# Kernel optimization log

Measured on AMD Instinct MI355X. Metric: run time of the kernel, lower is better.

## Reference

```python
import jax, jax.numpy as jnp
import numpy as np
import math

B, T, J, D2 = 32, 512, 43, 2
DM, H, FF, E, NC = 512, 8, 2048, 101, 100  # d_model, heads, ffn, n_experts(=max_output_len+1), classes


def _ln(x, g, b, eps=1e-5):
    mu = x.mean(-1, keepdims=True)
    var = ((x - mu) ** 2).mean(-1, keepdims=True)
    return (x - mu) / jnp.sqrt(var + eps) * g + b


def _pos_encoding(t, d):
    pos = jnp.arange(t, dtype=jnp.float32)[:, None]
    div = jnp.exp(jnp.arange(0, d, 2, dtype=jnp.float32) * (-math.log(10000.0) / d))
    pe = jnp.zeros((t, d), dtype=jnp.float32)
    pe = pe.at[:, 0::2].set(jnp.sin(pos * div))
    pe = pe.at[:, 1::2].set(jnp.cos(pos * div))
    return pe


def _mha(x, qkv_w, qkv_b, ow, ob, heads):
    b_, t_, d_ = x.shape
    dh = d_ // heads
    qkv = x @ qkv_w.T + qkv_b
    q, k, v = jnp.split(qkv, 3, axis=-1)
    sh = lambda a: a.reshape(b_, t_, heads, dh).transpose(0, 2, 1, 3)
    q, k, v = sh(q), sh(k), sh(v)
    s = jnp.einsum('bhqd,bhkd->bhqk', q, k) / jnp.sqrt(jnp.asarray(dh, x.dtype))
    a = jax.nn.softmax(s, axis=-1)
    ctx = jnp.einsum('bhqk,bhkd->bhqd', a, v).transpose(0, 2, 1, 3).reshape(b_, t_, d_)
    return ctx @ ow.T + ob


def _conv1d(x, w, b):  # x: [B,C,T], w: [O,I,3]
    y = jax.lax.conv_general_dilated(x, w, (1,), [(1, 1)], dimension_numbers=('NCH', 'OIH', 'NCH'))
    return y + b[None, :, None]


def _avgpool2(x):  # [B,C,T] -> [B,C,T//2]
    b_, c_, t_ = x.shape
    return x.reshape(b_, c_, t_ // 2, 2).mean(-1)


def _expert(pos, qkv_w, qkv_b, ow, ob, ng, nb, lw, lb, memory):
    m = memory + pos  # pos: [D], broadcast over [B,Tp,D]
    out = _mha(m, qkv_w, qkv_b, ow, ob, heads=1)
    c = out.mean(axis=1)           # [B,D]
    c = _ln(c, ng, nb)
    return c @ lw.T + lb           # [B,D]


_experts_vmapped = jax.vmap(_expert, in_axes=(0,) * 9 + (None,))


def _forward(poses, W_in, b_in,
             eq_w, eq_b, eo_w, eo_b, ef1_w, ef1_b, ef2_w, ef2_b,
             en1_g, en1_b, en2_g, en2_b,
             c1_w, c1_b, c2_w, c2_b, mlp_w, mlp_b,
             xp_pos, xp_qkv_w, xp_qkv_b, xp_o_w, xp_o_b, xp_n_g, xp_n_b, xp_l_w, xp_l_b,
             fn_g, fn_b, hd_w, hd_b):
    b_, t_, j_, d2_ = poses.shape
    x = poses.reshape(b_, t_, j_ * d2_)
    x = x @ W_in.T + b_in                          # [B,T,DM]
    x = x + _pos_encoding(t_, DM)[None]
    # 2-layer post-norm transformer encoder (torch default: relu FFN, norm after residual)
    for i in range(2):
        a = _mha(x, eq_w[i], eq_b[i], eo_w[i], eo_b[i], heads=H)
        x = _ln(x + a, en1_g[i], en1_b[i])
        ff = jax.nn.relu(x @ ef1_w[i].T + ef1_b[i]) @ ef2_w[i].T + ef2_b[i]
        x = _ln(x + ff, en2_g[i], en2_b[i])
    # temporal pooling: conv-gelu-pool x2  -> [B,DM,T/4]
    y = x.transpose(0, 2, 1)
    y = _avgpool2(jax.nn.gelu(_conv1d(y, c1_w, c1_b), approximate=False))
    y = _avgpool2(jax.nn.gelu(_conv1d(y, c2_w, c2_b), approximate=False))
    mem = y.transpose(0, 2, 1)                      # [B,T/4,DM]
    mem = jax.nn.gelu(mem @ mlp_w.T + mlp_b, approximate=False)
    # all position experts in one batched call: [E,B,DM]
    ctx = _experts_vmapped(xp_pos, xp_qkv_w, xp_qkv_b, xp_o_w, xp_o_b,
                           xp_n_g, xp_n_b, xp_l_w, xp_l_b, mem)
    ctx = _ln(ctx, fn_g, fn_b)
    logits = ctx @ hd_w.T + hd_b                    # [E,B,NC]
    return logits.transpose(1, 0, 2)                # [B,E,NC]


def setup_inputs() -> dict:
    key = jax.random.key(0)
    ks = iter(jax.random.split(key, 64))
    nrm = lambda shape, s=0.02: jax.random.normal(next(ks), shape, dtype=jnp.float32) * s
    inp = {
        'poses': jax.random.normal(next(ks), (B, T, J, D2), dtype=jnp.float32),
        'W_in': nrm((DM, J * D2)), 'b_in': jnp.zeros((DM,)),
        'eq_w': nrm((2, 3 * DM, DM)), 'eq_b': jnp.zeros((2, 3 * DM)),
        'eo_w': nrm((2, DM, DM)), 'eo_b': jnp.zeros((2, DM)),
        'ef1_w': nrm((2, FF, DM)), 'ef1_b': jnp.zeros((2, FF)),
        'ef2_w': nrm((2, DM, FF)), 'ef2_b': jnp.zeros((2, DM)),
        'en1_g': jnp.ones((2, DM)), 'en1_b': jnp.zeros((2, DM)),
        'en2_g': jnp.ones((2, DM)), 'en2_b': jnp.zeros((2, DM)),
        'c1_w': nrm((DM, DM, 3)), 'c1_b': jnp.zeros((DM,)),
        'c2_w': nrm((DM, DM, 3)), 'c2_b': jnp.zeros((DM,)),
        'mlp_w': nrm((DM, DM)), 'mlp_b': jnp.zeros((DM,)),
        'xp_pos': nrm((E, DM)),
        'xp_qkv_w': nrm((E, 3 * DM, DM)), 'xp_qkv_b': jnp.zeros((E, 3 * DM)),
        'xp_o_w': nrm((E, DM, DM)), 'xp_o_b': jnp.zeros((E, DM)),
        'xp_n_g': jnp.ones((E, DM)), 'xp_n_b': jnp.zeros((E, DM)),
        'xp_l_w': nrm((E, DM, DM)), 'xp_l_b': jnp.zeros((E, DM)),
        'fn_g': jnp.ones((DM,)), 'fn_b': jnp.zeros((DM,)),
        'hd_w': nrm((NC, DM)), 'hd_b': jnp.zeros((NC,)),
    }
    return inp


def reference(poses, W_in, b_in,
              eq_w, eq_b, eo_w, eo_b, ef1_w, ef1_b, ef2_w, ef2_b,
              en1_g, en1_b, en2_g, en2_b,
              c1_w, c1_b, c2_w, c2_b, mlp_w, mlp_b,
              xp_pos, xp_qkv_w, xp_qkv_b, xp_o_w, xp_o_b, xp_n_g, xp_n_b, xp_l_w, xp_l_b,
              fn_g, fn_b, hd_w, hd_b):
    return _forward(poses, W_in, b_in,
                    eq_w, eq_b, eo_w, eo_b, ef1_w, ef1_b, ef2_w, ef2_b,
                    en1_g, en1_b, en2_g, en2_b,
                    c1_w, c1_b, c2_w, c2_b, mlp_w, mlp_b,
                    xp_pos, xp_qkv_w, xp_qkv_b, xp_o_w, xp_o_b, xp_n_g, xp_n_b, xp_l_w, xp_l_b,
                    fn_g, fn_b, hd_w, hd_b)
```

## Files before the change

### kernel.cpp

```cpp
#include <hip/hip_runtime.h>
#include <math.h>

typedef unsigned short u16;
typedef __bf16 bf16_t;
typedef bf16_t bf16x8 __attribute__((ext_vector_type(8)));
typedef float f32x4v __attribute__((ext_vector_type(4)));
typedef u16 u16x8 __attribute__((ext_vector_type(8)));
typedef u16 u16x4 __attribute__((ext_vector_type(4)));

__device__ inline u16 f2bf(float f){ __bf16 h=(__bf16)f; return __builtin_bit_cast(u16,h); }
__device__ inline float bf2f(u16 u){ unsigned int x=((unsigned int)u)<<16; return __builtin_bit_cast(float,x); }

#define GLD16(gp,lp) __builtin_amdgcn_global_load_lds( \
  (const __attribute__((address_space(1))) void*)(gp), \
  (__attribute__((address_space(3))) void*)(lp), 16, 0, 0)

#define MFMA_B16(a,b,c) __builtin_amdgcn_mfma_f32_16x16x32_bf16(a,b,c,0,0,0)
#define ALPHA_S 0.044194173824159216f

struct GP {
  const u16* A; int lda; long long sA1, sA2;
  const u16* B; int ldb; long long sB1, sB2;
  const float* bias; long long sb1, sb2, sbg;
  float* Cf; u16* Cb; int ldc; long long sC1, sC2;
  int M, N, K, Z2, epi, perm;
  float alpha;
};

__device__ inline float epiF(float v,int epi){
  if(epi==1) return fmaxf(v,0.f);
  if(epi==2) return 0.5f*v*(1.f+erff(v*0.70710678118654752f));
  return v;
}

__global__ __launch_bounds__(256) void gemm_bt(GP p){
  __shared__ u16 L[3*8192];
  const int z=blockIdx.z, z1=z/p.Z2, z2=z-z1*p.Z2;
  const u16* __restrict__ Ab = p.A + z1*p.sA1 + z2*p.sA2;
  const u16* __restrict__ Bb = p.B + z1*p.sB1 + z2*p.sB2;
  const int tm=blockIdx.x*128, tn=blockIdx.y*128;
  const int t=threadIdx.x, lane=t&63, wv=t>>6;
  const int wr=(wv>>1)*64, wc=(wv&1)*64;
  const int fr=lane&15, c16=lane>>4;

  long long aoff[2], boff[2];
  #pragma unroll
  for(int q=0;q<2;q++){
    int s=(wv*2+q)*64+lane;
    int r=s>>2;
    int col=((s&3)^((r>>1)&3))*8;
    int ga=tm+r; if(ga>p.M-1) ga=p.M-1;
    int gb=tn+r; if(gb>p.N-1) gb=p.N-1;
    aoff[q]=(long long)ga*p.lda+col;
    boff[q]=(long long)gb*p.ldb+col;
  }

  auto STAGE=[&](int tk,int buf){
    const long long kk=(long long)tk*32;
    u16* base=&L[buf*8192];
    #pragma unroll
    for(int q=0;q<2;q++){
      GLD16(Ab+aoff[q]+kk, base+(wv*2+q)*512);
      GLD16(Bb+boff[q]+kk, base+4096+(wv*2+q)*512);
    }
  };

  const int nt = p.K >> 5;
  f32x4v acc[4][4]={};

  STAGE(0,0);
  if(nt>1){
    STAGE(1,1);
    asm volatile("s_waitcnt vmcnt(4)" ::: "memory");
  } else {
    asm volatile("s_waitcnt vmcnt(0)" ::: "memory");
  }
  __builtin_amdgcn_s_barrier();
  __builtin_amdgcn_sched_barrier(0);

  for(int i=0;i<nt;++i){
    const int buf=i%3;
    if(i+2<nt) STAGE(i+2,(i+2)%3);
    const u16* Abuf=&L[buf*8192];
    const u16* Bbuf=&L[buf*8192+4096];
    bf16x8 af[4], bfv[4];
    #pragma unroll
    for(int m=0;m<4;m++){ int r=wr+16*m+fr; af[m]=*(const bf16x8*)&Abuf[r*32+((c16^((r>>1)&3))*8)]; }
    #pragma unroll
    for(int n=0;n<4;n++){ int r=wc+16*n+fr; bfv[n]=*(const bf16x8*)&Bbuf[r*32+((c16^((r>>1)&3))*8)]; }
    #pragma unroll
    for(int m=0;m<4;m++)
      #pragma unroll
      for(int n=0;n<4;n++)
        acc[m][n]=MFMA_B16(af[m],bfv[n],acc[m][n]);
    if(i+1<nt){
      if(i+2<nt) asm volatile("s_waitcnt vmcnt(4)" ::: "memory");
      else       asm volatile("s_waitcnt vmcnt(0)" ::: "memory");
      __builtin_amdgcn_s_barrier();
      __builtin_amdgcn_sched_barrier(0);
    }
  }

  const int rq=lane>>4;
  const long long cbase = z1*p.sC1 + z2*p.sC2;
  float* __restrict__ Cf = p.Cf? p.Cf+cbase : nullptr;
  u16*  __restrict__ Cbp = p.Cb? p.Cb+cbase : nullptr;

  const bool vec = (!p.perm) && (p.epi!=3) && ((p.N&63)==0) && !(Cf&&Cbp);
  if(vec){
    float bvn[4];
    #pragma unroll
    for(int n=0;n<4;n++){
      int gc=tn+wc+n*16+fr; if(gc>p.N-1) gc=p.N-1;
      bvn[n]=p.bias? p.bias[z1*p.sb1+z2*p.sb2+(long long)gc*p.sbg] : 0.f;
    }
    if(Cbp){
      u16* my=(u16*)L + wv*1024;
      #pragma unroll
      for(int m=0;m<4;m++){
        __syncthreads();
        #pragma unroll
        for(int n=0;n<4;n++){
          int pg=((n^rq)<<4)+fr;
          #pragma unroll
          for(int r=0;r<4;r++)
            my[(4*rq+r)*64+pg]=f2bf(epiF(acc[m][n][r]*p.alpha+bvn[n],p.epi));
        }
        __syncthreads();
        #pragma unroll
        for(int ps=0;ps<2;ps++){
          int row=ps*8+(lane>>3), h=lane&7;
          int grow=tm+wr+m*16+row, gc0=tn+wc+h*8;
          if(grow<p.M && gc0<p.N){
            int phys=(((h>>1)^(row>>2))<<4)+((h&1)<<3);
            *(u16x8*)&Cbp[(long long)grow*p.ldc+gc0]=*(const u16x8*)&my[row*64+phys];
          }
        }
      }
    } else {
      float* my=(float*)L + wv*1024;
      #pragma unroll
      for(int m=0;m<4;m++){
        __syncthreads();
        #pragma unroll
        for(int n=0;n<4;n++){
          int pg=((n^rq)<<4)+fr;
          #pragma unroll
          for(int r=0;r<4;r++)
            my[(4*rq+r)*64+pg]=epiF(acc[m][n][r]*p.alpha+bvn[n],p.epi);
        }
        __syncthreads();
        #pragma unroll
        for(int ps=0;ps<2;ps++){
          int row=ps*8+(lane>>3), h=lane&7;
          int grow=tm+wr+m*16+row, gc0=tn+wc+h*8;
          if(grow<p.M && gc0<p.N){
            int phys=(((h>>1)^(row>>2))<<4)+((h&1)<<3);
            *(float4*)&Cf[(long long)grow*p.ldc+gc0]  =*(const float4*)&my[row*64+phys];
            *(float4*)&Cf[(long long)grow*p.ldc+gc0+4]=*(const float4*)&my[row*64+phys+4];
          }
        }
      }
    }
    return;
  }

  #pragma unroll
  for(int m=0;m<4;m++){
    int grow0=tm+wr+16*m+4*rq;
    #pragma unroll
    for(int n=0;n<4;n++){
      int gcol=tn+wc+16*n+fr;
      if(gcol>=p.N) continue;
      float bv = p.bias? p.bias[z1*p.sb1+z2*p.sb2+(long long)gcol*p.sbg] : 0.f;
      #pragma unroll
      for(int r=0;r<4;r++){
        int grow=grow0+r;
        if(grow>=p.M) continue;
        float v=acc[m][n][r]*p.alpha+bv;
        if(p.epi==1) v=fmaxf(v,0.f);
        else if(p.epi==2) v=0.5f*v*(1.f+erff(v*0.70710678118654752f));
        else if(p.epi==3){
          int tt=grow&511;
          float ang=(float)tt*expf((float)(gcol&~1)*(-0.017988946039015967f));
          v += (gcol&1)? cosf(ang) : sinf(ang);
        }
        long long ci;
        if(p.perm) ci = ((long long)((grow&31)*101 + (grow>>5)))*100 + gcol;
        else       ci = (long long)grow*p.ldc+gcol;
        if(Cf) Cf[ci]=v;
        if(Cbp) Cbp[ci]=f2bf(v);
      }
    }
  }
}

__global__ __launch_bounds__(256) void gemm_sfused(
    const u16* __restrict__ Pm, const u16* __restrict__ mem,
    const float* __restrict__ U, float* __restrict__ abar){
  __shared__ float Sl[128*129];
  u16* L=(u16*)Sl;
  const int z=blockIdx.x, e=z>>5, b=z&31;
  const u16* __restrict__ Ab = Pm + (long long)e*2097152 + (long long)b*65536;
  const u16* __restrict__ Bb = mem + (long long)b*65536;
  const int t=threadIdx.x, lane=t&63, wv=t>>6;
  const int wr=(wv>>1)*64, wc=(wv&1)*64;
  const int fr=lane&15, c16=lane>>4;

  long long aoff[2], boff[2];
  #pragma unroll
  for(int q=0;q<2;q++){
    int s=(wv*2+q)*64+lane;
    int r=s>>2;
    int col=((s&3)^((r>>1)&3))*8;
    aoff[q]=(long long)r*512+col;
    boff[q]=(long long)r*512+col;
  }
  auto STAGE=[&](int tk,int buf){
    const long long kk=(long long)tk*32;
    u16* base=&L[buf*8192];
    #pragma unroll
    for(int q=0;q<2;q++){
      GLD16(Ab+aoff[q]+kk, base+(wv*2+q)*512);
      GLD16(Bb+boff[q]+kk, base+4096+(wv*2+q)*512);
    }
  };

  f32x4v acc[4][4]={};
  STAGE(0,0);
  STAGE(1,1);
  asm volatile("s_waitcnt vmcnt(4)" ::: "memory");
  __builtin_amdgcn_s_barrier();
  __builtin_amdgcn_sched_barrier(0);

  for(int i=0;i<16;++i){
    const int buf=i%3;
    if(i+2<16) STAGE(i+2,(i+2)%3);
    const u16* Abuf=&L[buf*8192];
    const u16* Bbuf=&L[buf*8192+4096];
    bf16x8 af[4], bfv[4];
    #pragma unroll
    for(int m=0;m<4;m++){ int r=wr+16*m+fr; af[m]=*(const bf16x8*)&Abuf[r*32+((c16^((r>>1)&3))*8)]; }
    #pragma unroll
    for(int n=0;n<4;n++){ int r=wc+16*n+fr; bfv[n]=*(const bf16x8*)&Bbuf[r*32+((c16^((r>>1)&3))*8)]; }
    #pragma unroll
    for(int m=0;m<4;m++)
      #pragma unroll
      for(int n=0;n<4;n++)
        acc[m][n]=MFMA_B16(af[m],bfv[n],acc[m][n]);
    if(i+1<16){
      if(i+2<16) asm volatile("s_waitcnt vmcnt(4)" ::: "memory");
      else       asm volatile("s_waitcnt vmcnt(0)" ::: "memory");
      __builtin_amdgcn_s_barrier();
      __builtin_amdgcn_sched_barrier(0);
    }
  }

  const int rq=lane>>4;
  float bvn[4];
  #pragma unroll
  for(int n=0;n<4;n++){
    int col=wc+n*16+fr;
    bvn[n]=U[((long long)(b*128+col))*101+e];
  }
  __syncthreads();
  #pragma unroll
  for(int m=0;m<4;m++)
    #pragma unroll
    for(int n=0;n<4;n++){
      int col=wc+n*16+fr;
      #pragma unroll
      for(int r=0;r<4;r++){
        int row=wr+m*16+4*rq+r;
        Sl[row*129+col]=acc[m][n][r]*ALPHA_S+bvn[n];
      }
    }
  __syncthreads();
  {
    int row=t>>1, h=t&1;
    float* pr=&Sl[row*129+h*64];
    float mx=pr[0];
    for(int j=1;j<64;j++) mx=fmaxf(mx,pr[j]);
    mx=fmaxf(mx,__shfl_xor(mx,1));
    float s=0.f;
    for(int j=0;j<64;j++){ float ex=__expf(pr[j]-mx); pr[j]=ex; s+=ex; }
    s+=__shfl_xor(s,1);
    float inv=1.f/s;
    for(int j=0;j<64;j++) pr[j]*=inv;
  }
  __syncthreads();
  if(t<128){
    float s=0.f;
    for(int r=0;r<128;r++) s+=Sl[r*129+t];
    abar[(long long)z*128+t]=s*(1.f/128.f);
  }
}

__global__ __launch_bounds__(512) void gemm_big8(GP p){
  __shared__ u16 L[65536];
  const int z=blockIdx.z, z1=z/p.Z2, z2=z-z1*p.Z2;
  const u16* __restrict__ Ab = p.A + z1*p.sA1 + z2*p.sA2;
  const u16* __restrict__ Bb = p.B + z1*p.sB1 + z2*p.sB2;
  const int tm=blockIdx.x*256, tn=blockIdx.y*256;
  const int t=threadIdx.x, lane=t&63, wv=t>>6;
  const int wr2=(wv>>2)*128, wc2=(wv&3)*64;
  const int fr=lane&15, c16=lane>>4;

  long long aoff[2], boff[2];
  {
    int rr=t>>2, cs=((t&3)^((t>>3)&3))*8;
    #pragma unroll
    for(int q=0;q<2;q++){
      int ga=tm+q*128+rr; if(ga>p.M-1) ga=p.M-1;
      int gb=tn+q*128+rr; if(gb>p.N-1) gb=p.N-1;
      aoff[q]=(long long)ga*p.lda+cs;
      boff[q]=(long long)gb*p.ldb+cs;
    }
  }

  auto STAGE_A=[&](int kt,int d,int ks){
    const long long k0=(long long)kt*64+ks*32;
    u16* dst=&L[d*16384+ks*8192];
    GLD16(Ab+aoff[0]+k0, dst+t*8);
    GLD16(Ab+aoff[1]+k0, dst+4096+t*8);
  };
  auto STAGE_B=[&](int kt,int d,int ks){
    const long long k0=(long long)kt*64+ks*32;
    u16* dst=&L[32768+d*16384+ks*8192];
    GLD16(Bb+boff[0]+k0, dst+t*8);
    GLD16(Bb+boff[1]+k0, dst+4096+t*8);
  };
  auto LDA_=[&](int d,int ks,int m)->bf16x8{
    int R=wr2+m*16+fr;
    return *(const bf16x8*)&L[d*16384+ks*8192+R*32+((c16^((R>>1)&3))*8)];
  };
  auto LDB_=[&](int d,int ks,int n)->bf16x8{
    int R=wc2+n*16+fr;
    return *(const bf16x8*)&L[32768+d*16384+ks*8192+R*32+((c16^((R>>1)&3))*8)];
  };

  const int ntk=p.K>>6;
  f32x4v acc[8][4]={};
  bf16x8 af[8], bq0, bq1, bq2, bq3;

  STAGE_A(0,0,0); STAGE_B(0,0,0); STAGE_A(0,0,1); STAGE_B(0,0,1);
  asm volatile("s_waitcnt vmcnt(4)" ::: "memory");
  __builtin_amdgcn_s_barrier();
  __builtin_amdgcn_sched_barrier(0);

  for(int kt=0;kt<ntk;++kt){
    const int d=kt&1, nd=d^1;
    const bool nxt=(kt+1<ntk);
    #pragma unroll
    for(int m=0;m<8;m++) af[m]=LDA_(d,0,m);
    bq0=LDB_(d,0,0); bq1=LDB_(d,0,1);
    if(nxt) STAGE_A(kt+1,nd,0);
    __builtin_amdgcn_s_barrier();
    asm volatile("s_waitcnt lgkmcnt(0)" ::: "memory");
    __builtin_amdgcn_sched_barrier(0);
    __builtin_amdgcn_s_setprio(1);
    #pragma unroll
    for(int m=0;m<8;m++){
      acc[m][0]=MFMA_B16(af[m],bq0,acc[m][0]);
      acc[m][1]=MFMA_B16(af[m],bq1,acc[m][1]);
    }
    __builtin_amdgcn_s_setprio(0);
    __builtin_amdgcn_s_barrier();
    bq2=LDB_(d,0,2); bq3=LDB_(d,0,3);
    if(nxt) STAGE_B(kt+1,nd,0);
    __builtin_amdgcn_s_barrier();
    asm volatile("s_waitcnt lgkmcnt(0)" ::: "memory");
    __builtin_amdgcn_sched_barrier(0);
    __builtin_amdgcn_s_setprio(1);
    #pragma unroll
    for(int m=0;m<8;m++){
      acc[m][2]=MFMA_B16(af[m],bq2,acc[m][2]);
      acc[m][3]=MFMA_B16(af[m],bq3,acc[m][3]);
    }
    __builtin_amdgcn_s_setprio(0);
    if(nxt) asm volatile("s_waitcnt vmcnt(4)" ::: "memory");
    else    asm volatile("s_waitcnt vmcnt(0)" ::: "memory");
    __builtin_amdgcn_s_barrier();
    __builtin_amdgcn_sched_barrier(0);
    #pragma unroll
    for(int m=0;m<8;m++) af[m]=LDA_(d,1,m);
    bq0=LDB_(d,1,0); bq1=LDB_(d,1,1);
    if(nxt) STAGE_A(kt+1,nd,1);
    __builtin_amdgcn_s_barrier();
    asm volatile("s_waitcnt lgkmcnt(0)" ::: "memory");
    __builtin_amdgcn_sched_barrier(0);
    __builtin_amdgcn_s_setprio(1);
    #pragma unroll
    for(int m=0;m<8;m++){
      acc[m][0]=MFMA_B16(af[m],bq0,acc[m][0]);
      acc[m][1]=MFMA_B16(af[m],bq1,acc[m][1]);
    }
    __builtin_amdgcn_s_setprio(0);
    __builtin_amdgcn_s_barrier();
    bq2=LDB_(d,1,2); bq3=LDB_(d,1,3);
    if(nxt) STAGE_B(kt+1,nd,1);
    __builtin_amdgcn_s_barrier();
    asm volatile("s_waitcnt lgkmcnt(0)" ::: "memory");
    __builtin_amdgcn_sched_barrier(0);
    __builtin_amdgcn_s_setprio(1);
    #pragma unroll
    for(int m=0;m<8;m++){
      acc[m][2]=MFMA_B16(af[m],bq2,acc[m][2]);
      acc[m][3]=MFMA_B16(af[m],bq3,acc[m][3]);
    }
    __builtin_amdgcn_s_setprio(0);
    if(nxt) asm volatile("s_waitcnt vmcnt(4)" ::: "memory");
    __builtin_amdgcn_s_barrier();
    __builtin_amdgcn_sched_barrier(0);
  }

  const int rq=lane>>4;
  const long long cbase = z1*p.sC1 + z2*p.sC2;
  float* __restrict__ Cf = p.Cf? p.Cf+cbase : nullptr;
  u16*  __restrict__ Cbp = p.Cb? p.Cb+cbase : nullptr;

  const bool vec = (!p.perm) && (p.epi!=3) && ((p.N&63)==0) && !(Cf&&Cbp);
  if(vec){
    float bvn[4];
    #pragma unroll
    for(int n=0;n<4;n++){
      int gc=tn+wc2+n*16+fr; if(gc>p.N-1) gc=p.N-1;
      bvn[n]=p.bias? p.bias[z1*p.sb1+z2*p.sb2+(long long)gc*p.sbg] : 0.f;
    }
    if(Cbp){
      u16* my=(u16*)L + wv*1024;
      #pragma unroll
      for(int m=0;m<8;m++){
        __syncthreads();
        #pragma unroll
        for(int n=0;n<4;n++){
          int pg=((n^rq)<<4)+fr;
          #pragma unroll
          for(int r=0;r<4;r++)
            my[(4*rq+r)*64+pg]=f2bf(epiF(acc[m][n][r]*p.alpha+bvn[n],p.epi));
        }
        __syncthreads();
        #pragma unroll
        for(int ps=0;ps<2;ps++){
          int row=ps*8+(lane>>3), h=lane&7;
          int grow=tm+wr2+m*16+row, gc0=tn+wc2+h*8;
          if(grow<p.M && gc0<p.N){
            int phys=(((h>>1)^(row>>2))<<4)+((h&1)<<3);
            *(u16x8*)&Cbp[(long long)grow*p.ldc+gc0]=*(const u16x8*)&my[row*64+phys];
          }
        }
      }
    } else {
      float* my=(float*)L + wv*1024;
      #pragma unroll
      for(int m=0;m<8;m++){
        __syncthreads();
        #pragma unroll
        for(int n=0;n<4;n++){
          int pg=((n^rq)<<4)+fr;
          #pragma unroll
          for(int r=0;r<4;r++)
            my[(4*rq+r)*64+pg]=epiF(acc[m][n][r]*p.alpha+bvn[n],p.epi);
        }
        __syncthreads();
        #pragma unroll
        for(int ps=0;ps<2;ps++){
          int row=ps*8+(lane>>3), h=lane&7;
          int grow=tm+wr2+m*16+row, gc0=tn+wc2+h*8;
          if(grow<p.M && gc0<p.N){
            int phys=(((h>>1)^(row>>2))<<4)+((h&1)<<3);
            *(float4*)&Cf[(long long)grow*p.ldc+gc0]  =*(const float4*)&my[row*64+phys];
            *(float4*)&Cf[(long long)grow*p.ldc+gc0+4]=*(const float4*)&my[row*64+phys+4];
          }
        }
      }
    }
    return;
  }

  #pragma unroll
  for(int m=0;m<8;m++){
    int grow0=tm+wr2+m*16+4*rq;
    #pragma unroll
    for(int n=0;n<4;n++){
      int gcol=tn+wc2+n*16+fr;
      if(gcol>=p.N) continue;
      float bv = p.bias? p.bias[z1*p.sb1+z2*p.sb2+gcol] : 0.f;
      #pragma unroll
      for(int r=0;r<4;r++){
        int grow=grow0+r;
        if(grow>=p.M) continue;
        float v=epiF(acc[m][n][r]*p.alpha+bv,p.epi);
        long long ci=(long long)grow*p.ldc+gcol;
        if(Cf) Cf[ci]=v;
        if(Cbp) Cbp[ci]=f2bf(v);
      }
    }
  }
}

__global__ __launch_bounds__(256) void softmax512b(u16* __restrict__ S, int nrows){
  int row=blockIdx.x*4+(threadIdx.x>>6);
  if(row>=nrows) return;
  int lane=threadIdx.x&63;
  u16* p=S+(long long)row*512;
  u16x8 raw=*(u16x8*)&p[lane*8];
  float f[8];
  #pragma unroll
  for(int j=0;j<8;j++) f[j]=bf2f(raw[j]);
  float m=f[0];
  #pragma unroll
  for(int j=1;j<8;j++) m=fmaxf(m,f[j]);
  #pragma unroll
  for(int off=32;off;off>>=1) m=fmaxf(m,__shfl_xor(m,off));
  float s=0.f;
  #pragma unroll
  for(int j=0;j<8;j++){ f[j]=__expf(f[j]-m); s+=f[j]; }
  #pragma unroll
  for(int off=32;off;off>>=1) s+=__shfl_xor(s,off);
  float inv=1.f/s;
  u16x8 o;
  #pragma unroll
  for(int j=0;j<8;j++) o[j]=f2bf(f[j]*inv);
  *(u16x8*)&p[lane*8]=o;
}

__global__ __launch_bounds__(256) void ln512(
    const float* __restrict__ x, const float* __restrict__ res,
    const float* __restrict__ g, const float* __restrict__ bb, int pergroup,
    float* __restrict__ outf, u16* __restrict__ outb, int nrows)
{
  int row=blockIdx.x*4+(threadIdx.x>>6);
  if(row>=nrows) return;
  int lane=threadIdx.x&63;
  const float4* xp=(const float4*)(x+(long long)row*512);
  float4 v0=xp[lane], v1=xp[lane+64];
  if(res){
    const float4* rp=(const float4*)(res+(long long)row*512);
    float4 w0=rp[lane], w1=rp[lane+64];
    v0.x+=w0.x; v0.y+=w0.y; v0.z+=w0.z; v0.w+=w0.w;
    v1.x+=w1.x; v1.y+=w1.y; v1.z+=w1.z; v1.w+=w1.w;
  }
  float s=v0.x+v0.y+v0.z+v0.w+v1.x+v1.y+v1.z+v1.w;
  #pragma unroll
  for(int off=32;off;off>>=1) s+=__shfl_xor(s,off);
  float mu=s*(1.f/512.f);
  float q=(v0.x-mu)*(v0.x-mu)+(v0.y-mu)*(v0.y-mu)+(v0.z-mu)*(v0.z-mu)+(v0.w-mu)*(v0.w-mu)
        +(v1.x-mu)*(v1.x-mu)+(v1.y-mu)*(v1.y-mu)+(v1.z-mu)*(v1.z-mu)+(v1.w-mu)*(v1.w-mu);
  #pragma unroll
  for(int off=32;off;off>>=1) q+=__shfl_xor(q,off);
  float rstd=rsqrtf(q*(1.f/512.f)+1e-5f);
  long long go = pergroup? (long long)(row>>5)*512 : 0;
  float4 g0=((const float4*)(g+go))[lane],  g1=((const float4*)(g+go))[lane+64];
  float4 b0=((const float4*)(bb+go))[lane], b1=((const float4*)(bb+go))[lane+64];
  float4 o0,o1;
  o0.x=(v0.x-mu)*rstd*g0.x+b0.x; o0.y=(v0.y-mu)*rstd*g0.y+b0.y;
  o0.z=(v0.z-mu)*rstd*g0.z+b0.z; o0.w=(v0.w-mu)*rstd*g0.w+b0.w;
  o1.x=(v1.x-mu)*rstd*g1.x+b1.x; o1.y=(v1.y-mu)*rstd*g1.y+b1.y;
  o1.z=(v1.z-mu)*rstd*g1.z+b1.z; o1.w=(v1.w-mu)*rstd*g1.w+b1.w;
  if(outf){
    ((float4*)(outf+(long long)row*512))[lane]=o0;
    ((float4*)(outf+(long long)row*512))[lane+64]=o1;
  }
  if(outb){
    u16x4 h0,h1;
    h0[0]=f2bf(o0.x); h0[1]=f2bf(o0.y); h0[2]=f2bf(o0.z); h0[3]=f2bf(o0.w);
    h1[0]=f2bf(o1.x); h1[1]=f2bf(o1.y); h1[2]=f2bf(o1.z); h1[3]=f2bf(o1.w);
    ((u16x4*)(outb+(long long)row*512))[lane]=h0;
    ((u16x4*)(outb+(long long)row*512))[lane+64]=h1;
  }
}

__global__ __launch_bounds__(256) void vtransb(const u16* __restrict__ qkv,
                                               u16* __restrict__ Vt){
  __shared__ u16 tile[64][72];
  int tt=blockIdx.x, h=blockIdx.y, zb=blockIdx.z;
  int t=threadIdx.x;
  int i=t>>2, j0=(t&3)*16;
  const u16* src = qkv + ((long long)(zb*512 + tt*64 + i))*1536 + 1024 + h*64 + j0;
  *(u16x8*)&tile[i][j0]   = *(const u16x8*)&src[0];
  *(u16x8*)&tile[i][j0+8] = *(const u16x8*)&src[8];
  __syncthreads();
  int j=t>>2, i0=(t&3)*16;
  u16 tmp[16];
  #pragma unroll
  for(int c=0;c<16;c++) tmp[c]=tile[i0+c][j];
  u16* dst = Vt + ((long long)((zb*8+h)*64 + j))*512 + tt*64 + i0;
  *(u16x8*)&dst[0]=*(u16x8*)&tmp[0];
  *(u16x8*)&dst[8]=*(u16x8*)&tmp[8];
}

__global__ __launch_bounds__(256) void trcvtb(const float* __restrict__ src,
                                              u16* __restrict__ dst){
  __shared__ float tile[64][65];
  int bi=blockIdx.x, bj=blockIdx.y, z=blockIdx.z;
  int e=z>>1, half=z&1;
  const float* s = src + (long long)e*786432 + half*262144;
  int t=threadIdx.x;
  int i=t>>2, j0=(t&3)*16;
  const float* sp = s + (long long)(bi*64+i)*512 + bj*64 + j0;
  #pragma unroll
  for(int c=0;c<4;c++){
    float4 v=((const float4*)sp)[c];
    tile[i][j0+4*c+0]=v.x; tile[i][j0+4*c+1]=v.y;
    tile[i][j0+4*c+2]=v.z; tile[i][j0+4*c+3]=v.w;
  }
  __syncthreads();
  int j=t>>2, i0=(t&3)*16;
  u16* d = dst + (long long)z*262144 + (long long)(bj*64+j)*512 + bi*64 + i0;
  u16x8 o0,o1;
  #pragma unroll
  for(int c=0;c<8;c++){ o0[c]=f2bf(tile[i0+c][j]); o1[c]=f2bf(tile[i0+8+c][j]); }
  *(u16x8*)&d[0]=o0; *(u16x8*)&d[8]=o1;
}

__global__ __launch_bounds__(256) void im2col3b(const u16* __restrict__ in,
                                                u16* __restrict__ out,
                                                int Tlen, long long n8){
  long long idx=(long long)blockIdx.x*256+threadIdx.x;
  if(idx>=n8) return;
  int i8=(int)(idx&63); long long s=idx>>6;
  int dt=(int)(s%3); long long bt=s/3;
  int tt=(int)(bt%Tlen); int b=(int)(bt/Tlen);
  int tsrc=tt+dt-1;
  u16x8 v={0,0,0,0,0,0,0,0};
  if(tsrc>=0 && tsrc<Tlen) v=*(const u16x8*)&in[((long long)(b*Tlen+tsrc))*512 + i8*8];
  *(u16x8*)&out[idx*8]=v;
}

__global__ __launch_bounds__(256) void wrepackb(const float* __restrict__ w,
                                                u16* __restrict__ out){
  int idx=blockIdx.x*256+threadIdx.x;
  if(idx>=512*1536) return;
  int o=idx/1536; int rem=idx-o*1536;
  int dt=rem/512; int i=rem-dt*512;
  out[idx]=f2bf(w[((long long)o*512+i)*3+dt]);
}

__global__ __launch_bounds__(256) void pool2b(const float* __restrict__ in,
                                              u16* __restrict__ out,
                                              int Tlen, long long n4){
  long long idx=(long long)blockIdx.x*256+threadIdx.x;
  if(idx>=n4) return;
  int c=(int)((idx&127)*4); long long s=idx>>7;
  int half=Tlen/2;
  int tp=(int)(s%half); int b=(int)(s/half);
  const float* p=in+((long long)(b*Tlen+2*tp))*512+c;
  float4 a=*(const float4*)p, d=*(const float4*)(p+512);
  u16x4 o;
  o[0]=f2bf(0.5f*(a.x+d.x)); o[1]=f2bf(0.5f*(a.y+d.y));
  o[2]=f2bf(0.5f*(a.z+d.z)); o[3]=f2bf(0.5f*(a.w+d.w));
  *(u16x4*)&out[(s*512)+c]=o;
}

__global__ __launch_bounds__(256) void cvt_bf16(const float* __restrict__ in,
                                                u16* __restrict__ out, long long n8){
  long long i=(long long)blockIdx.x*256+threadIdx.x;
  if(i>=n8) return;
  const float4* p=(const float4*)(in+i*8);
  float4 a=p[0], b=p[1];
  u16x8 o;
  o[0]=f2bf(a.x); o[1]=f2bf(a.y); o[2]=f2bf(a.z); o[3]=f2bf(a.w);
  o[4]=f2bf(b.x); o[5]=f2bf(b.y); o[6]=f2bf(b.z); o[7]=f2bf(b.w);
  *(u16x8*)(out+i*8)=o;
}

__global__ __launch_bounds__(256) void cvt_wv(const float* __restrict__ in,
                                              u16* __restrict__ out, long long n8){
  long long idx=(long long)blockIdx.x*256+threadIdx.x;
  if(idx>=n8) return;
  int e=(int)(idx>>15); long long r8=idx&32767;
  const float* p=in+(long long)e*786432+524288+r8*8;
  float4 a=((const float4*)p)[0], b=((const float4*)p)[1];
  u16x8 o;
  o[0]=f2bf(a.x); o[1]=f2bf(a.y); o[2]=f2bf(a.z); o[3]=f2bf(a.w);
  o[4]=f2bf(b.x); o[5]=f2bf(b.y); o[6]=f2bf(b.z); o[7]=f2bf(b.w);
  *(u16x8*)(out+idx*8)=o;
}

__global__ __launch_bounds__(256) void cvt_pad(const float* __restrict__ in,
                                               u16* __restrict__ out,
                                               int rows, int ks, int kd){
  long long idx=(long long)blockIdx.x*256+threadIdx.x;
  if(idx>=(long long)rows*kd) return;
  int r=(int)(idx/kd), c=(int)(idx-(long long)r*kd);
  out[idx]=(c<ks)? f2bf(in[(long long)r*ks+c]) : (u16)0;
}

__global__ __launch_bounds__(256) void expert_reduce2(
    const float* __restrict__ abar, const u16* __restrict__ mem,
    const float* __restrict__ pos, u16* __restrict__ wout)
{
  int b=blockIdx.x, e=blockIdx.y;
  int t=threadIdx.x;
  __shared__ float abf[128];
  if(t<128) abf[t]=abar[((long long)(e*32+b))*128+t];
  __syncthreads();
  float c0=0.f, c1=0.f;
  const u16* mb = mem + (long long)b*65536;
  for(int k=0;k<128;++k){
    float a=abf[k];
    c0+=a*bf2f(mb[k*512+t]);
    c1+=a*bf2f(mb[k*512+t+256]);
  }
  c0+=pos[(long long)e*512+t]; c1+=pos[(long long)e*512+t+256];
  u16* o=wout+((long long)e*32+b)*512;
  o[t]=f2bf(c0); o[t+256]=f2bf(c1);
}

static inline int ceildiv(int a,int b){return (a+b-1)/b;}

static GP mkGP(const u16* A,int lda,long long sA1,long long sA2,
  const u16* B,int ldb,long long sB1,long long sB2,
  const float* bias,long long sb1,long long sb2,
  float* Cf,u16* Cb,int ldc,long long sC1,long long sC2,
  int M,int N,int K,int Z2,int epi,float alpha,long long sbg,int perm){
  GP p;
  p.A=A; p.lda=lda; p.sA1=sA1; p.sA2=sA2;
  p.B=B; p.ldb=ldb; p.sB1=sB1; p.sB2=sB2;
  p.bias=bias; p.sb1=sb1; p.sb2=sb2; p.sbg=sbg;
  p.Cf=Cf; p.Cb=Cb; p.ldc=ldc; p.sC1=sC1; p.sC2=sC2;
  p.M=M; p.N=N; p.K=K; p.Z2=Z2; p.epi=epi; p.perm=perm; p.alpha=alpha;
  return p;
}

static void gemmB(hipStream_t s,
  const u16* A,int lda,long long sA1,long long sA2,
  const u16* B,int ldb,long long sB1,long long sB2,
  const float* bias,long long sb1,long long sb2,
  float* Cf,u16* Cb,int ldc,long long sC1,long long sC2,
  int M,int N,int K,int Z,int Z2,int epi,float alpha,
  long long sbg=1,int perm=0){
  GP p=mkGP(A,lda,sA1,sA2,B,ldb,sB1,sB2,bias,sb1,sb2,Cf,Cb,ldc,sC1,sC2,M,N,K,Z2,epi,alpha,sbg,perm);
  dim3 g(ceildiv(M,128), ceildiv(N,128), Z);
  gemm_bt<<<g, dim3(256), 0, s>>>(p);
}

static void gemmBig(hipStream_t s,
  const u16* A,int lda,long long sA1,long long sA2,
  const u16* B,int ldb,long long sB1,long long sB2,
  const float* bias,long long sb1,long long sb2,
  float* Cf,u16* Cb,int ldc,long long sC1,long long sC2,
  int M,int N,int K,int Z,int Z2,int epi,float alpha){
  GP p=mkGP(A,lda,sA1,sA2,B,ldb,sB1,sB2,bias,sb1,sb2,Cf,Cb,ldc,sC1,sC2,M,N,K,Z2,epi,alpha,1,0);
  dim3 g(ceildiv(M,256), ceildiv(N,256), Z);
  gemm_big8<<<g, dim3(512), 0, s>>>(p);
}

static inline void cvt(hipStream_t s, const float* in, u16* out, long long n){
  long long n8=n/8;
  cvt_bf16<<<(int)((n8+255)/256),256,0,s>>>(in,out,n8);
}

extern "C" void kernel_launch(void* const* d_in, const int* in_sizes, int n_in,
                              void* d_out, int out_size, void* d_ws, size_t ws_size,
                              hipStream_t stream) {
  (void)in_sizes; (void)n_in; (void)out_size;
  const float* poses=(const float*)d_in[0];
  const float* W_in =(const float*)d_in[1];
  const float* b_in =(const float*)d_in[2];
  const float* eq_w =(const float*)d_in[3];
  const float* eq_b =(const float*)d_in[4];
  const float* eo_w =(const float*)d_in[5];
  const float* eo_b =(const float*)d_in[6];
  const float* ef1_w=(const float*)d_in[7];
  const float* ef1_b=(const float*)d_in[8];
  const float* ef2_w=(const float*)d_in[9];
  const float* ef2_b=(const float*)d_in[10];
  const float* en1_g=(const float*)d_in[11];
  const float* en1_b=(const float*)d_in[12];
  const float* en2_g=(const float*)d_in[13];
  const float* en2_b=(const float*)d_in[14];
  const float* c1_w =(const float*)d_in[15];
  const float* c1_b =(const float*)d_in[16];
  const float* c2_w =(const float*)d_in[17];
  const float* c2_b =(const float*)d_in[18];
  const float* mlp_w=(const float*)d_in[19];
  const float* mlp_b=(const float*)d_in[20];
  const float* xp_pos  =(const float*)d_in[21];
  const float* xp_qkv_w=(const float*)d_in[22];
  const float* xp_qkv_b=(const float*)d_in[23];
  const float* xp_o_w  =(const float*)d_in[24];
  const float* xp_o_b  =(const float*)d_in[25];
  const float* xp_n_g  =(const float*)d_in[26];
  const float* xp_n_b  =(const float*)d_in[27];
  const float* xp_l_w  =(const float*)d_in[28];
  const float* xp_l_b  =(const float*)d_in[29];
  const float* fn_g =(const float*)d_in[30];
  const float* fn_b =(const float*)d_in[31];
  const float* hd_w =(const float*)d_in[32];
  const float* hd_b =(const float*)d_in[33];
  float* out=(float*)d_out;

  float* ws=(float*)d_ws;
  size_t off=0;
  auto alloc=[&](size_t n)->float*{ float* p=ws+off; off+=(n+255)&~(size_t)255; return p; };
  float* RA = alloc(137760768);
  float* RB = alloc(84381184);
  float* RC = alloc(5849088);
  if(off*sizeof(float) > ws_size) return;

  u16* qkvb =(u16*)RA;
  u16* Sb16 =(u16*)(RA+12582912);
  u16* ffb  =(u16*)(RA+46137344);
  u16* ctxb =(u16*)(RA+62914560);
  u16* Vtb  =(u16*)(RA+67108864);
  float* act0f=RA+71303168;
  float* act1f=RA+79691776;
  float* tmpf =RA+88080384;
  u16* act0b=(u16*)(RA+96468992);
  u16* act1b=(u16*)(RA+98566144);
  u16* Pb   =(u16*)RA;
  float* abarf=RA+105906176;
  float* U  =RA+132382720;
  float* ctx1=RA+132796416;
  float* ctx2=RA+134451200;
  u16* ln1b =(u16*)(RA+136105984);
  u16* ln2b =(u16*)(RA+136933376);
  u16* posesb=(u16*)RB;
  u16* W_inb =(u16*)(RB+786432);
  u16* eqwb  =(u16*)(RB+811008);
  u16* eowb  =(u16*)(RB+1597440);
  u16* ef1wb =(u16*)(RB+1859584);
  u16* ef2wb =(u16*)(RB+2908160);
  u16* wc1b  =(u16*)(RB+3956736);
  u16* wc2b  =(u16*)(RB+4349952);
  u16* mlpwb =(u16*)(RB+4743168);
  u16* hdwb  =(u16*)(RB+4874240);
  u16* xposb =(u16*)(RB+4899840);
  u16* owb   =(u16*)(RB+4925696);
  u16* lwb   =(u16*)(RB+18163968);
  u16* wvb   =(u16*)(RB+31402240);
  u16* wqkT  =(u16*)(RB+44640512);
  u16* Gpb   =(u16*)(RB+71117056);
  u16* Hb    =(u16*)(RB+84355328);
  u16* gmemb =(u16*)RC;
  u16* p1b   =(u16*)(RC+1048576);
  u16* membb =(u16*)(RC+3145728);
  u16* wb    =(u16*)(RC+4194304);
  u16* cmeanb=(u16*)(RC+5021696);

  cvt_pad<<<ceildiv(16384*96,256),256,0,stream>>>(poses,posesb,16384,86,96);
  cvt_pad<<<ceildiv(512*96,256),256,0,stream>>>(W_in,W_inb,512,86,96);
  cvt(stream,eq_w,eqwb,1572864);
  cvt(stream,eo_w,eowb,524288);
  cvt(stream,ef1_w,ef1wb,2097152);
  cvt(stream,ef2_w,ef2wb,2097152);
  cvt(stream,mlp_w,mlpwb,262144);
  cvt(stream,hd_w,hdwb,51200);
  cvt(stream,xp_pos,xposb,51712);
  cvt(stream,xp_o_w,owb,26476544);
  cvt(stream,xp_l_w,lwb,26476544);
  wrepackb<<<ceildiv(512*1536,256),256,0,stream>>>(c1_w,wc1b);
  wrepackb<<<ceildiv(512*1536,256),256,0,stream>>>(c2_w,wc2b);
  trcvtb<<<dim3(8,8,202),256,0,stream>>>(xp_qkv_w,wqkT);
  cvt_wv<<<ceildiv(101*32768,256),256,0,stream>>>(xp_qkv_w,wvb,(long long)101*32768);

  gemmB(stream, posesb,96,0,0, W_inb,96,0,0, b_in,0,0,
        act0f,act0b,512,0,0, 16384,512,96, 1,1, 3,1.f);

  for(int l=0;l<2;++l){
    gemmBig(stream, act0b,512,0,0, eqwb+(long long)l*786432,512,0,0,
          eq_b+(long long)l*1536,0,0, nullptr,qkvb,1536,0,0, 16384,1536,512, 1,1, 0,1.f);
    gemmB(stream, qkvb,1536,786432,64, qkvb+512,1536,786432,64, nullptr,0,0,
          nullptr,Sb16,512,2097152,262144, 512,512,64, 256,8, 0,0.125f);
    softmax512b<<<32768,256,0,stream>>>(Sb16,131072);
    vtransb<<<dim3(8,8,32),256,0,stream>>>(qkvb,Vtb);
    gemmB(stream, Sb16,512,2097152,262144, Vtb,512,262144,32768, nullptr,0,0,
          nullptr,ctxb,512,262144,64, 512,64,512, 256,8, 0,1.f);
    gemmBig(stream, ctxb,512,0,0, eowb+(long long)l*262144,512,0,0,
          eo_b+(long long)l*512,0,0, tmpf,nullptr,512,0,0, 16384,512,512, 1,1, 0,1.f);
    ln512<<<4096,256,0,stream>>>(tmpf,act0f,en1_g+(long long)l*512,en1_b+(long long)l*512,0,
                                 act1f,act1b,16384);
    gemmBig(stream, act1b,512,0,0, ef1wb+(long long)l*1048576,512,0,0,
          ef1_b+(long long)l*2048,0,0, nullptr,ffb,2048,0,0, 16384,2048,512, 1,1, 1,1.f);
    gemmBig(stream, ffb,2048,0,0, ef2wb+(long long)l*1048576,2048,0,0,
          ef2_b+(long long)l*512,0,0, tmpf,nullptr,512,0,0, 16384,512,2048, 1,1, 0,1.f);
    ln512<<<4096,256,0,stream>>>(tmpf,act1f,en2_g+(long long)l*512,en2_b+(long long)l*512,0,
                                 act0f,act0b,16384);
  }

  u16* Ccb=(u16*)RA;
  im2col3b<<<(int)(((long long)16384*1536/8+255)/256),256,0,stream>>>(act0b,Ccb,512,(long long)16384*1536/8);
  gemmBig(stream, Ccb,1536,0,0, wc1b,1536,0,0, c1_b,0,0,
        tmpf,nullptr,512,0,0, 16384,512,1536, 1,1, 2,1.f);
  pool2b<<<(int)(((long long)32*256*128+255)/256),256,0,stream>>>(tmpf,p1b,512,(long long)32*256*128);
  im2col3b<<<(int)(((long long)8192*1536/8+255)/256),256,0,stream>>>(p1b,Ccb,256,(long long)8192*1536/8);
  gemmBig(stream, Ccb,1536,0,0, wc2b,1536,0,0, c2_b,0,0,
        tmpf,nullptr,512,0,0, 8192,512,1536, 1,1, 2,1.f);
  pool2b<<<(int)(((long long)32*128*128+255)/256),256,0,stream>>>(tmpf,membb,256,(long long)32*128*128);
  gemmBig(stream, membb,512,0,0, mlpwb,512,0,0, mlp_b,0,0,
        nullptr,gmemb,512,0,0, 4096,512,512, 1,1, 2,1.f);

  gemmBig(stream, wqkT+262144,512,524288,0, wqkT,512,524288,0, nullptr,0,0,
        nullptr,Gpb,512,262144,0, 512,512,512, 101,1, 0,1.f);
  gemmB(stream, Gpb,512,262144,0, xposb,512,512,0, nullptr,0,0,
        nullptr,Hb,1,512,0, 512,1,512, 101,1, 0,1.f);
  gemmB(stream, gmemb,512,0,0, Hb,512,0,0, nullptr,0,0,
        U,nullptr,101,0,0, 4096,101,512, 1,1, 0,ALPHA_S);
  gemmBig(stream, gmemb,512,0,0, Gpb,512,262144,0, nullptr,0,0,
        nullptr,Pb,512,2097152,0, 4096,512,512, 101,1, 0,1.f);
  gemm_sfused<<<3232,256,0,stream>>>(Pb, gmemb, U, abarf);
  expert_reduce2<<<dim3(32,101),256,0,stream>>>(abarf,gmemb,xp_pos,wb);
  gemmB(stream, wb,512,16384,0, wvb,512,262144,0, xp_qkv_b+1024,1536,0,
        nullptr,cmeanb,512,16384,0, 32,512,512, 101,1, 0,1.f);

  gemmB(stream, cmeanb,512,16384,0, owb,512,262144,0, xp_o_b,512,0,
        ctx1,nullptr,512,16384,0, 32,512,512, 101,1, 0,1.f);
  ln512<<<808,256,0,stream>>>(ctx1,nullptr,xp_n_g,xp_n_b,1, nullptr,ln1b,3232);
  gemmB(stream, ln1b,512,16384,0, lwb,512,262144,0, xp_l_b,512,0,
        ctx2,nullptr,512,16384,0, 32,512,512, 101,1, 0,1.f);
  ln512<<<808,256,0,stream>>>(ctx2,nullptr,fn_g,fn_b,0, nullptr,ln2b,3232);
  gemmB(stream, ln2b,512,0,0, hdwb,512,0,0, hd_b,0,0,
        out,nullptr,100,0,0, 3232,100,512, 1,1, 0,1.f, 1,1);
}
```

Measured before the change: 2.028 ms.

## Remap GEMM workgroups per XCD and vectorize fused softmax LDS access

```diff
diff --git a/kernel.cpp b/kernel.cpp
--- a/kernel.cpp
+++ b/kernel.cpp
@@ -33,12 +33,23 @@
   return v;
 }
 
+__device__ inline void xcd_remap(int& bx,int& by,int& bz){
+  int gx=gridDim.x, gy=gridDim.y;
+  int nwg=gx*gy*gridDim.z;
+  int flat=blockIdx.x+gx*(blockIdx.y+gy*blockIdx.z);
+  int q=nwg>>3, r=nwg&7;
+  int xcd=flat&7, sub=flat>>3;
+  int wg=(xcd<r? xcd*(q+1) : r*(q+1)+(xcd-r)*q)+sub;
+  bx=wg%gx; int t2=wg/gx; by=t2%gy; bz=t2/gy;
+}
+
 __global__ __launch_bounds__(256) void gemm_bt(GP p){
   __shared__ u16 L[3*8192];
-  const int z=blockIdx.z, z1=z/p.Z2, z2=z-z1*p.Z2;
+  int bx,by,bz; xcd_remap(bx,by,bz);
+  const int z=bz, z1=z/p.Z2, z2=z-z1*p.Z2;
   const u16* __restrict__ Ab = p.A + z1*p.sA1 + z2*p.sA2;
   const u16* __restrict__ Bb = p.B + z1*p.sB1 + z2*p.sB2;
-  const int tm=blockIdx.x*128, tn=blockIdx.y*128;
+  const int tm=bx*128, tn=by*128;
   const int t=threadIdx.x, lane=t&63, wv=t>>6;
   const int wr=(wv>>1)*64, wc=(wv&1)*64;
   const int fr=lane&15, c16=lane>>4;
@@ -198,7 +209,7 @@
 __global__ __launch_bounds__(256) void gemm_sfused(
     const u16* __restrict__ Pm, const u16* __restrict__ mem,
     const float* __restrict__ U, float* __restrict__ abar){
-  __shared__ float Sl[128*129];
+  __shared__ float Sl[128*132];
   u16* L=(u16*)Sl;
   const int z=blockIdx.x, e=z>>5, b=z&31;
   const u16* __restrict__ Ab = Pm + (long long)e*2097152 + (long long)b*65536;
@@ -272,36 +283,53 @@
       #pragma unroll
       for(int r=0;r<4;r++){
         int row=wr+m*16+4*rq+r;
-        Sl[row*129+col]=acc[m][n][r]*ALPHA_S+bvn[n];
+        Sl[row*132+col]=acc[m][n][r]*ALPHA_S+bvn[n];
       }
     }
   __syncthreads();
   {
     int row=t>>1, h=t&1;
-    float* pr=&Sl[row*129+h*64];
-    float mx=pr[0];
-    for(int j=1;j<64;j++) mx=fmaxf(mx,pr[j]);
+    float4* p4=(float4*)&Sl[row*132+h*64];
+    float mx=-3.0e38f;
+    #pragma unroll 4
+    for(int j=0;j<16;j++){
+      float4 v=p4[j];
+      mx=fmaxf(mx,fmaxf(fmaxf(v.x,v.y),fmaxf(v.z,v.w)));
+    }
     mx=fmaxf(mx,__shfl_xor(mx,1));
     float s=0.f;
-    for(int j=0;j<64;j++){ float ex=__expf(pr[j]-mx); pr[j]=ex; s+=ex; }
+    #pragma unroll 4
+    for(int j=0;j<16;j++){
+      float4 v=p4[j];
+      v.x=__expf(v.x-mx); v.y=__expf(v.y-mx);
+      v.z=__expf(v.z-mx); v.w=__expf(v.w-mx);
+      s+=v.x+v.y+v.z+v.w;
+      p4[j]=v;
+    }
     s+=__shfl_xor(s,1);
     float inv=1.f/s;
-    for(int j=0;j<64;j++) pr[j]*=inv;
+    #pragma unroll 4
+    for(int j=0;j<16;j++){
+      float4 v=p4[j];
+      v.x*=inv; v.y*=inv; v.z*=inv; v.w*=inv;
+      p4[j]=v;
+    }
   }
   __syncthreads();
   if(t<128){
     float s=0.f;
-    for(int r=0;r<128;r++) s+=Sl[r*129+t];
+    for(int r=0;r<128;r++) s+=Sl[r*132+t];
     abar[(long long)z*128+t]=s*(1.f/128.f);
   }
 }
 
 __global__ __launch_bounds__(512) void gemm_big8(GP p){
   __shared__ u16 L[65536];
-  const int z=blockIdx.z, z1=z/p.Z2, z2=z-z1*p.Z2;
+  int bx,by,bz; xcd_remap(bx,by,bz);
+  const int z=bz, z1=z/p.Z2, z2=z-z1*p.Z2;
   const u16* __restrict__ Ab = p.A + z1*p.sA1 + z2*p.sA2;
   const u16* __restrict__ Bb = p.B + z1*p.sB1 + z2*p.sB2;
-  const int tm=blockIdx.x*256, tn=blockIdx.y*256;
+  const int tm=bx*256, tn=by*256;
   const int t=threadIdx.x, lane=t&63, wv=t>>6;
   const int wr2=(wv>>2)*128, wc2=(wv&3)*64;
   const int fr=lane&15, c16=lane>>4;
```

Result: slower. 2.078 ms (+2.4%).
